# Kernel optimization log

Measured on AMD Instinct MI355X. Metric: run time of the kernel, lower is better.

The kernel has to match this reference:

```python
import jax, jax.numpy as jnp
import numpy as np

WIN_H, WIN_W, DILATION = 3, 3, 1
EPS = 1e-12  # torch F.normalize eps


def setup_inputs() -> dict:
    key = jax.random.key(0)
    feature = jax.random.normal(key, (4, 32, 256, 512), dtype=jnp.float32)
    return {"feature": feature}


def reference(feature):
    B, C, H, W = feature.shape
    d = DILATION
    # L2 normalize over channel dim (torch F.normalize semantics)
    norm = jnp.sqrt(jnp.sum(feature * feature, axis=1, keepdims=True))
    feat = feature / jnp.maximum(norm, EPS)
    # pad spatial dims by dilation (matches nn.Unfold padding=dilation for 3x3)
    padded = jnp.pad(feat, ((0, 0), (0, 0), (d, d), (d, d)))
    center_idx = (WIN_H * WIN_W) // 2
    affs = []
    # fixed small 3x3 stencil loop; each slice is a shifted view, dot with center
    for k in range(WIN_H * WIN_W):
        if k == center_idx:
            continue
        i, j = k // WIN_W, k % WIN_W
        nb = jax.lax.dynamic_slice(padded, (0, 0, i * d, j * d), (B, C, H, W))
        affs.append(jnp.sum(nb * feat, axis=1))  # (B,H,W)
    affinity = jnp.stack(affs, axis=1)  # (B, 8, H, W)
    cut = jnp.float32(0.0)
    return jnp.where(affinity < cut, cut, affinity)
```

## Files before the change

kernel.cpp:

```cpp
#include <hip/hip_runtime.h>


#define AF_B 4
#define AF_C 32
#define AF_H 256
#define AF_W 512
#define AF_EPS 1e-12f
#define AF_PLANE ((size_t)AF_H * AF_W)

__global__ __launch_bounds__(256) void affinity_sym_kernel(const float* __restrict__ f,
                                                           float* __restrict__ out) {
    const int cpx = gridDim.x >> 3;
    const int bid = ((int)blockIdx.x & 7) * cpx + ((int)blockIdx.x >> 3);

    const int G = bid * 256 + (int)threadIdx.x;
    const int w0 = (G & 127) << 2;
    const int rowIdx = G >> 7;
    const int h = rowIdx & (AF_H - 1);
    const int b = rowIdx >> 8;

    const bool vS = (h + 1) < AF_H;
    const bool vR = (w0 + 4) < AF_W;
    const bool vL = w0 > 0;
    const float mS = vS ? 1.0f : 0.0f;
    const float mR = vR ? 1.0f : 0.0f;
    const float mRS = mR * mS;
    const float mLS = (vL ? 1.0f : 0.0f) * mS;
    const int offR = vR ? 4 : 0;
    const int offL = vL ? -1 : 0;

    const float* pc = f + (size_t)b * AF_C * AF_PLANE + (size_t)h * AF_W + w0;
    const float* ps = pc + (vS ? AF_W : 0);

    float ssq0=0,ssq1=0,ssq2=0,ssq3=0, ssqR=0;
    float nsq0=0,nsq1=0,nsq2=0,nsq3=0, nsqL=0,nsqR=0;
    float dE0=0,dE1=0,dE2=0,dE3=0;
    float dS0=0,dS1=0,dS2=0,dS3=0;
    float dSE0=0,dSE1=0,dSE2=0,dSE3=0;
    float dSW0=0,dSW1=0,dSW2=0,dSW3=0;

#pragma unroll
    for (int c = 0; c < AF_C; ++c) {
        const float4 cc = *(const float4*)pc;
        const float ccR = pc[offR] * mR;
        float4 cs = *(const float4*)ps;
        const float csR = ps[offR] * mRS;
        const float csL = ps[offL] * mLS;
        cs.x *= mS; cs.y *= mS; cs.z *= mS; cs.w *= mS;
        pc += AF_PLANE; ps += AF_PLANE;

        ssq0 += cc.x*cc.x; ssq1 += cc.y*cc.y; ssq2 += cc.z*cc.z; ssq3 += cc.w*cc.w;
        ssqR += ccR*ccR;
        nsq0 += cs.x*cs.x; nsq1 += cs.y*cs.y; nsq2 += cs.z*cs.z; nsq3 += cs.w*cs.w;
        nsqL += csL*csL;   nsqR += csR*csR;
        dE0 += cc.x*cc.y;  dE1 += cc.y*cc.z;  dE2 += cc.z*cc.w;  dE3 += cc.w*ccR;
        dS0 += cc.x*cs.x;  dS1 += cc.y*cs.y;  dS2 += cc.z*cs.z;  dS3 += cc.w*cs.w;
        dSE0 += cc.x*cs.y; dSE1 += cc.y*cs.z; dSE2 += cc.z*cs.w; dSE3 += cc.w*csR;
        dSW0 += cc.x*csL;  dSW1 += cc.y*cs.x; dSW2 += cc.z*cs.y; dSW3 += cc.w*cs.z;
    }

    const float ic0 = 1.0f / fmaxf(sqrtf(ssq0), AF_EPS);
    const float ic1 = 1.0f / fmaxf(sqrtf(ssq1), AF_EPS);
    const float ic2 = 1.0f / fmaxf(sqrtf(ssq2), AF_EPS);
    const float ic3 = 1.0f / fmaxf(sqrtf(ssq3), AF_EPS);
    const float icR = 1.0f / fmaxf(sqrtf(ssqR), AF_EPS);
    const float is0 = 1.0f / fmaxf(sqrtf(nsq0), AF_EPS);
    const float is1 = 1.0f / fmaxf(sqrtf(nsq1), AF_EPS);
    const float is2 = 1.0f / fmaxf(sqrtf(nsq2), AF_EPS);
    const float is3 = 1.0f / fmaxf(sqrtf(nsq3), AF_EPS);
    const float isL = 1.0f / fmaxf(sqrtf(nsqL), AF_EPS);
    const float isR = 1.0f / fmaxf(sqrtf(nsqR), AF_EPS);

    const float E0 = fmaxf(dE0*ic0*ic1, 0.0f);
    const float E1 = fmaxf(dE1*ic1*ic2, 0.0f);
    const float E2 = fmaxf(dE2*ic2*ic3, 0.0f);
    const float E3 = fmaxf(dE3*ic3*icR, 0.0f);
    const float S0 = fmaxf(dS0*ic0*is0, 0.0f);
    const float S1 = fmaxf(dS1*ic1*is1, 0.0f);
    const float S2 = fmaxf(dS2*ic2*is2, 0.0f);
    const float S3 = fmaxf(dS3*ic3*is3, 0.0f);
    const float SE0 = fmaxf(dSE0*ic0*is1, 0.0f);
    const float SE1 = fmaxf(dSE1*ic1*is2, 0.0f);
    const float SE2 = fmaxf(dSE2*ic2*is3, 0.0f);
    const float SE3 = fmaxf(dSE3*ic3*isR, 0.0f);
    const float SW0 = fmaxf(dSW0*ic0*isL, 0.0f);
    const float SW1 = fmaxf(dSW1*ic1*is0, 0.0f);
    const float SW2 = fmaxf(dSW2*ic2*is1, 0.0f);
    const float SW3 = fmaxf(dSW3*ic3*is2, 0.0f);

    float* ob = out + (size_t)b * 8 * AF_PLANE + (size_t)h * AF_W + w0;

    *(float4*)(ob + 4*AF_PLANE) = make_float4(E0,E1,E2,E3);
    *(float4*)(ob + 6*AF_PLANE) = make_float4(S0,S1,S2,S3);
    *(float4*)(ob + 7*AF_PLANE) = make_float4(SE0,SE1,SE2,SE3);
    *(float4*)(ob + 5*AF_PLANE) = make_float4(SW0,SW1,SW2,SW3);

    float* o3 = ob + 3*AF_PLANE;
    o3[1] = E0; o3[2] = E1; o3[3] = E2;
    if (vR) o3[4] = E3;
    if (!vL) o3[0] = 0.0f;

    if (vS) {
        float* on = ob + AF_W;
        *(float4*)(on + 1*AF_PLANE) = make_float4(S0,S1,S2,S3);
        float* o0 = on;
        o0[1] = SE0; o0[2] = SE1; o0[3] = SE2;
        if (vR) o0[4] = SE3;
        if (!vL) o0[0] = 0.0f;
        float* o2 = on + 2*AF_PLANE;
        if (vL) o2[-1] = SW0;
        o2[0] = SW1; o2[1] = SW2; o2[2] = SW3;
        if (!vR) o2[3] = 0.0f;
    }

    if (h == 0) {
        float* oz = out + (size_t)b * 8 * AF_PLANE + w0;
        const float4 z4 = make_float4(0.0f, 0.0f, 0.0f, 0.0f);
        *(float4*)(oz + 0*AF_PLANE) = z4;
        *(float4*)(oz + 1*AF_PLANE) = z4;
        *(float4*)(oz + 2*AF_PLANE) = z4;
    }
}

extern "C" void kernel_launch(void* const* d_in, const int* in_sizes, int n_in,
                              void* d_out, int out_size, void* d_ws, size_t ws_size,
                              hipStream_t stream) {
    const float* f = (const float*)d_in[0];
    float* out = (float*)d_out;
    affinity_sym_kernel<<<512, 256, 0, stream>>>(f, out);
}
```

Baseline: 24.88 us.

## Split channel reduction across lane groups and distribute output stores

Each wave now splits the 32-channel loop into four 8-channel groups held by different 16-lane groups, then combines the partial sums with cross-lane xor shuffles. The grid grows from 512 to 2048 blocks, and each block covers half of one row. Each channel group writes a different subset of the output planes, so stores are spread across lanes instead of all coming from one thread. The aim is more parallelism and memory-level concurrency for this bandwidth-bound kernel. The cost is 28 shuffle reductions per thread and narrower per-lane loads along w.

```diff
diff --git a/kernel.cpp b/kernel.cpp
--- a/kernel.cpp
+++ b/kernel.cpp
@@ -8,20 +8,30 @@
 #define AF_EPS 1e-12f
 #define AF_PLANE ((size_t)AF_H * AF_W)
 
-__global__ __launch_bounds__(256) void affinity_sym_kernel(const float* __restrict__ f,
-                                                           float* __restrict__ out) {
+__device__ __forceinline__ float redx(float v) {
+    v += __shfl_xor(v, 16, 64);
+    v += __shfl_xor(v, 32, 64);
+    return v;
+}
+
+__global__ __launch_bounds__(256, 8) void affinity_split_kernel(const float* __restrict__ f,
+                                                                float* __restrict__ out) {
     const int cpx = gridDim.x >> 3;
     const int bid = ((int)blockIdx.x & 7) * cpx + ((int)blockIdx.x >> 3);
+    const int whalf = bid & 1;
+    const int h = (bid >> 1) & (AF_H - 1);
+    const int b = bid >> 9;
 
-    const int G = bid * 256 + (int)threadIdx.x;
-    const int w0 = (G & 127) << 2;
-    const int rowIdx = G >> 7;
-    const int h = rowIdx & (AF_H - 1);
-    const int b = rowIdx >> 8;
+    const int tid = (int)threadIdx.x;
+    const int lane = tid & 63;
+    const int p = lane & 15;
+    const int cg = lane >> 4;
+    const int wv = tid >> 6;
+    const int w0 = (whalf << 8) + (((wv << 4) + p) << 2);
 
-    const bool vS = (h + 1) < AF_H;
     const bool vR = (w0 + 4) < AF_W;
     const bool vL = w0 > 0;
+    const bool vS = (h + 1) < AF_H;
     const float mS = vS ? 1.0f : 0.0f;
     const float mR = vR ? 1.0f : 0.0f;
     const float mRS = mR * mS;
@@ -29,7 +39,8 @@
     const int offR = vR ? 4 : 0;
     const int offL = vL ? -1 : 0;
 
-    const float* pc = f + (size_t)b * AF_C * AF_PLANE + (size_t)h * AF_W + w0;
+    const float* pc = f + ((size_t)b * AF_C + (size_t)(cg << 3)) * AF_PLANE
+                        + (size_t)h * AF_W + w0;
     const float* ps = pc + (vS ? AF_W : 0);
 
     float ssq0=0,ssq1=0,ssq2=0,ssq3=0, ssqR=0;
@@ -40,7 +51,7 @@
     float dSW0=0,dSW1=0,dSW2=0,dSW3=0;
 
 #pragma unroll
-    for (int c = 0; c < AF_C; ++c) {
+    for (int k = 0; k < 8; ++k) {
         const float4 cc = *(const float4*)pc;
         const float ccR = pc[offR] * mR;
         float4 cs = *(const float4*)ps;
@@ -58,6 +69,14 @@
         dSE0 += cc.x*cs.y; dSE1 += cc.y*cs.z; dSE2 += cc.z*cs.w; dSE3 += cc.w*csR;
         dSW0 += cc.x*csL;  dSW1 += cc.y*cs.x; dSW2 += cc.z*cs.y; dSW3 += cc.w*cs.z;
     }
+
+    ssq0=redx(ssq0); ssq1=redx(ssq1); ssq2=redx(ssq2); ssq3=redx(ssq3); ssqR=redx(ssqR);
+    nsq0=redx(nsq0); nsq1=redx(nsq1); nsq2=redx(nsq2); nsq3=redx(nsq3);
+    nsqL=redx(nsqL); nsqR=redx(nsqR);
+    dE0=redx(dE0);   dE1=redx(dE1);   dE2=redx(dE2);   dE3=redx(dE3);
+    dS0=redx(dS0);   dS1=redx(dS1);   dS2=redx(dS2);   dS3=redx(dS3);
+    dSE0=redx(dSE0); dSE1=redx(dSE1); dSE2=redx(dSE2); dSE3=redx(dSE3);
+    dSW0=redx(dSW0); dSW1=redx(dSW1); dSW2=redx(dSW2); dSW3=redx(dSW3);
 
     const float ic0 = 1.0f / fmaxf(sqrtf(ssq0), AF_EPS);
     const float ic1 = 1.0f / fmaxf(sqrtf(ssq1), AF_EPS);
@@ -89,36 +108,38 @@
     const float SW3 = fmaxf(dSW3*ic3*is2, 0.0f);
 
     float* ob = out + (size_t)b * 8 * AF_PLANE + (size_t)h * AF_W + w0;
+    float* oz = out + (size_t)b * 8 * AF_PLANE + w0;
+    const float4 z4 = make_float4(0.f, 0.f, 0.f, 0.f);
 
-    *(float4*)(ob + 4*AF_PLANE) = make_float4(E0,E1,E2,E3);
-    *(float4*)(ob + 6*AF_PLANE) = make_float4(S0,S1,S2,S3);
-    *(float4*)(ob + 7*AF_PLANE) = make_float4(SE0,SE1,SE2,SE3);
-    *(float4*)(ob + 5*AF_PLANE) = make_float4(SW0,SW1,SW2,SW3);
-
-    float* o3 = ob + 3*AF_PLANE;
-    o3[1] = E0; o3[2] = E1; o3[3] = E2;
-    if (vR) o3[4] = E3;
-    if (!vL) o3[0] = 0.0f;
-
-    if (vS) {
-        float* on = ob + AF_W;
-        *(float4*)(on + 1*AF_PLANE) = make_float4(S0,S1,S2,S3);
-        float* o0 = on;
-        o0[1] = SE0; o0[2] = SE1; o0[3] = SE2;
-        if (vR) o0[4] = SE3;
-        if (!vL) o0[0] = 0.0f;
-        float* o2 = on + 2*AF_PLANE;
-        if (vL) o2[-1] = SW0;
-        o2[0] = SW1; o2[1] = SW2; o2[2] = SW3;
-        if (!vR) o2[3] = 0.0f;
-    }
-
-    if (h == 0) {
-        float* oz = out + (size_t)b * 8 * AF_PLANE + w0;
-        const float4 z4 = make_float4(0.0f, 0.0f, 0.0f, 0.0f);
-        *(float4*)(oz + 0*AF_PLANE) = z4;
-        *(float4*)(oz + 1*AF_PLANE) = z4;
-        *(float4*)(oz + 2*AF_PLANE) = z4;
+    if (cg == 0) {
+        *(float4*)(ob + 4*AF_PLANE) = make_float4(E0, E1, E2, E3);
+        float* o3 = ob + 3*AF_PLANE;
+        o3[1] = E0; o3[2] = E1; o3[3] = E2;
+        if (vR) o3[4] = E3;
+        if (!vL) o3[0] = 0.0f;
+        if (h == 0) *(float4*)(oz + 0*AF_PLANE) = z4;
+    } else if (cg == 1) {
+        *(float4*)(ob + 5*AF_PLANE) = make_float4(SW0, SW1, SW2, SW3);
+        if (vS) {
+            float* o2 = ob + AF_W + 2*AF_PLANE;
+            if (vL) o2[-1] = SW0;
+            o2[0] = SW1; o2[1] = SW2; o2[2] = SW3;
+            if (!vR) o2[3] = 0.0f;
+        }
+        if (h == 0) *(float4*)(oz + 1*AF_PLANE) = z4;
+    } else if (cg == 2) {
+        *(float4*)(ob + 6*AF_PLANE) = make_float4(S0, S1, S2, S3);
+        if (vS)
+            *(float4*)(ob + AF_W + 1*AF_PLANE) = make_float4(S0, S1, S2, S3);
+        if (h == 0) *(float4*)(oz + 2*AF_PLANE) = z4;
+    } else {
+        *(float4*)(ob + 7*AF_PLANE) = make_float4(SE0, SE1, SE2, SE3);
+        if (vS) {
+            float* o0 = ob + AF_W;
+            o0[1] = SE0; o0[2] = SE1; o0[3] = SE2;
+            if (vR) o0[4] = SE3;
+            if (!vL) o0[0] = 0.0f;
+        }
     }
 }
 
@@ -127,5 +148,5 @@
                               hipStream_t stream) {
     const float* f = (const float*)d_in[0];
     float* out = (float*)d_out;
-    affinity_sym_kernel<<<512, 256, 0, stream>>>(f, out);
+    affinity_split_kernel<<<2048, 256, 0, stream>>>(f, out);
 }
```

New measurement: 26.57 us. +6.8%, slower.

## Batch channel loads in groups of 8 and use wave shuffles for halo values

Applied to the files above, without the earlier changes.

The channel loop now runs in groups of 8: all float4 loads for a group are issued up front, and a sched_barrier keeps them ahead of the math so more memory requests are in flight per thread. Neighbor halo elements (right, and left of the south row) now come from lane shuffles within the 64-wide wave. Global loads for them happen only on edge lanes, replacing the scalar extra loads every thread issued before. In exchange the kernel uses more registers, which can lower occupancy, and adds shuffle instructions.

```diff
diff --git a/kernel.cpp b/kernel.cpp
--- a/kernel.cpp
+++ b/kernel.cpp
@@ -7,27 +7,27 @@
 #define AF_W 512
 #define AF_EPS 1e-12f
 #define AF_PLANE ((size_t)AF_H * AF_W)
+#define CB 8
 
-__global__ __launch_bounds__(256) void affinity_sym_kernel(const float* __restrict__ f,
+__global__ __launch_bounds__(256) void affinity_mlp_kernel(const float* __restrict__ f,
                                                            float* __restrict__ out) {
     const int cpx = gridDim.x >> 3;
     const int bid = ((int)blockIdx.x & 7) * cpx + ((int)blockIdx.x >> 3);
 
-    const int G = bid * 256 + (int)threadIdx.x;
+    const int tid = (int)threadIdx.x;
+    const int G = bid * 256 + tid;
     const int w0 = (G & 127) << 2;
     const int rowIdx = G >> 7;
     const int h = rowIdx & (AF_H - 1);
     const int b = rowIdx >> 8;
+    const int lane = tid & 63;
 
     const bool vS = (h + 1) < AF_H;
     const bool vR = (w0 + 4) < AF_W;
     const bool vL = w0 > 0;
     const float mS = vS ? 1.0f : 0.0f;
-    const float mR = vR ? 1.0f : 0.0f;
-    const float mRS = mR * mS;
-    const float mLS = (vL ? 1.0f : 0.0f) * mS;
-    const int offR = vR ? 4 : 0;
-    const int offL = vL ? -1 : 0;
+    const bool bR = (lane == 63) && vR;
+    const bool bL = (lane == 0) && vL;
 
     const float* pc = f + (size_t)b * AF_C * AF_PLANE + (size_t)h * AF_W + w0;
     const float* ps = pc + (vS ? AF_W : 0);
@@ -40,23 +40,45 @@
     float dSW0=0,dSW1=0,dSW2=0,dSW3=0;
 
 #pragma unroll
-    for (int c = 0; c < AF_C; ++c) {
-        const float4 cc = *(const float4*)pc;
-        const float ccR = pc[offR] * mR;
-        float4 cs = *(const float4*)ps;
-        const float csR = ps[offR] * mRS;
-        const float csL = ps[offL] * mLS;
-        cs.x *= mS; cs.y *= mS; cs.z *= mS; cs.w *= mS;
-        pc += AF_PLANE; ps += AF_PLANE;
+    for (int gb = 0; gb < AF_C / CB; ++gb) {
+        float4 cc[CB], cs[CB];
+        float eR[CB], eS[CB], eL[CB];
+#pragma unroll
+        for (int k = 0; k < CB; ++k) {
+            const float* p = pc + (size_t)k * AF_PLANE;
+            const float* q = ps + (size_t)k * AF_PLANE;
+            cc[k] = *(const float4*)p;
+            cs[k] = *(const float4*)q;
+            eR[k] = bR ? p[4]  : 0.0f;
+            eS[k] = bR ? q[4]  : 0.0f;
+            eL[k] = bL ? q[-1] : 0.0f;
+        }
+        __builtin_amdgcn_sched_barrier(0);
 
-        ssq0 += cc.x*cc.x; ssq1 += cc.y*cc.y; ssq2 += cc.z*cc.z; ssq3 += cc.w*cc.w;
-        ssqR += ccR*ccR;
-        nsq0 += cs.x*cs.x; nsq1 += cs.y*cs.y; nsq2 += cs.z*cs.z; nsq3 += cs.w*cs.w;
-        nsqL += csL*csL;   nsqR += csR*csR;
-        dE0 += cc.x*cc.y;  dE1 += cc.y*cc.z;  dE2 += cc.z*cc.w;  dE3 += cc.w*ccR;
-        dS0 += cc.x*cs.x;  dS1 += cc.y*cs.y;  dS2 += cc.z*cs.z;  dS3 += cc.w*cs.w;
-        dSE0 += cc.x*cs.y; dSE1 += cc.y*cs.z; dSE2 += cc.z*cs.w; dSE3 += cc.w*csR;
-        dSW0 += cc.x*csL;  dSW1 += cc.y*cs.x; dSW2 += cc.z*cs.y; dSW3 += cc.w*cs.z;
+#pragma unroll
+        for (int k = 0; k < CB; ++k) {
+            const float sh_ccx = __shfl(cc[k].x, lane + 1);
+            const float sh_csx = __shfl(cs[k].x, lane + 1);
+            const float sh_csw = __shfl(cs[k].w, lane - 1);
+
+            const float ccx = cc[k].x, ccy = cc[k].y, ccz = cc[k].z, ccw = cc[k].w;
+            const float ccR = (lane == 63) ? eR[k] : sh_ccx;
+            const float csx = cs[k].x * mS, csy = cs[k].y * mS,
+                        csz = cs[k].z * mS, csw = cs[k].w * mS;
+            const float csR = ((lane == 63) ? eS[k] : sh_csx) * mS;
+            const float csL = ((lane == 0)  ? eL[k] : sh_csw) * mS;
+
+            ssq0 += ccx*ccx; ssq1 += ccy*ccy; ssq2 += ccz*ccz; ssq3 += ccw*ccw;
+            ssqR += ccR*ccR;
+            nsq0 += csx*csx; nsq1 += csy*csy; nsq2 += csz*csz; nsq3 += csw*csw;
+            nsqL += csL*csL; nsqR += csR*csR;
+            dE0 += ccx*ccy;  dE1 += ccy*ccz;  dE2 += ccz*ccw;  dE3 += ccw*ccR;
+            dS0 += ccx*csx;  dS1 += ccy*csy;  dS2 += ccz*csz;  dS3 += ccw*csw;
+            dSE0 += ccx*csy; dSE1 += ccy*csz; dSE2 += ccz*csw; dSE3 += ccw*csR;
+            dSW0 += ccx*csL; dSW1 += ccy*csx; dSW2 += ccz*csy; dSW3 += ccw*csz;
+        }
+        pc += (size_t)CB * AF_PLANE;
+        ps += (size_t)CB * AF_PLANE;
     }
 
     const float ic0 = 1.0f / fmaxf(sqrtf(ssq0), AF_EPS);
@@ -127,5 +149,5 @@
                               hipStream_t stream) {
     const float* f = (const float*)d_in[0];
     float* out = (float*)d_out;
-    affinity_sym_kernel<<<512, 256, 0, stream>>>(f, out);
+    affinity_mlp_kernel<<<512, 256, 0, stream>>>(f, out);
 }
```

After: 27.60 us. 1.11x slower.
